# Kernel optimization log

Measured on AMD Instinct MI355X. Metric: run time of the kernel, lower is better.

The kernel has to match this reference:

```python
import jax, jax.numpy as jnp
import numpy as np

EPS = 1e-5
H = 12  # num_heads

def ste_sign(x):
    # forward: sign(x) in {-1,+1}; backward: grad passes where |x|<1 (clip STE)
    c = jnp.clip(x, -1.0, 1.0)
    s = jnp.where(x >= 0, 1.0, -1.0).astype(x.dtype)
    return c + jax.lax.stop_gradient(s - c)

def bin_w(w):
    # adaptive per-output-channel scaling: alpha = mean|w| (detached), weight = alpha*sign(w)
    alpha = jax.lax.stop_gradient(jnp.mean(jnp.abs(w), axis=1, keepdims=True))
    return alpha * ste_sign(w)

def layernorm(x, g, b):
    mu = jnp.mean(x, axis=-1, keepdims=True)
    var = jnp.var(x, axis=-1, keepdims=True)
    return (x - mu) * jax.lax.rsqrt(var + EPS) * g + b

def setup_inputs():
    key = jax.random.key(0)
    ks = jax.random.split(key, 6)
    B, N, C, hid = 8, 1024, 768, 3072
    s = 0.02
    return {
        "x": jax.random.normal(ks[0], (B, N, C), jnp.float32),
        "ln1_g": jnp.ones((C,), jnp.float32),
        "ln1_b": jnp.zeros((C,), jnp.float32),
        "w_qkv": jax.random.normal(ks[1], (3 * C, C), jnp.float32) * s,
        "w_proj": jax.random.normal(ks[2], (C, C), jnp.float32) * s,
        "b_proj": jnp.zeros((C,), jnp.float32),
        "ls1_g": 1e-5 * jnp.ones((C,), jnp.float32),
        "ln2_g": jnp.ones((C,), jnp.float32),
        "ln2_b": jnp.zeros((C,), jnp.float32),
        "w_fc1": jax.random.normal(ks[3], (hid, C), jnp.float32) * s,
        "b_fc1": jnp.zeros((hid,), jnp.float32),
        "w_fc2": jax.random.normal(ks[4], (C, hid), jnp.float32) * s,
        "b_fc2": jnp.zeros((C,), jnp.float32),
        "ls2_g": 1e-5 * jnp.ones((C,), jnp.float32),
    }

def reference(x, ln1_g, ln1_b, w_qkv, w_proj, b_proj, ls1_g, ln2_g, ln2_b, w_fc1, b_fc1, w_fc2, b_fc2, ls2_g):
    B, N, C = x.shape
    hd = C // H
    scale = hd ** -0.5
    # --- binarized attention ---
    h = layernorm(x, ln1_g, ln1_b)
    qkv = jnp.einsum('bnc,oc->bno', ste_sign(h), bin_w(w_qkv))        # 1w1a qkv proj
    qkv = qkv.reshape(B, N, 3, H, hd).transpose(2, 0, 3, 1, 4)        # [3,B,H,N,hd]
    bqkv = ste_sign(qkv)                                              # BinaryQuantizer
    q, k, v = bqkv[0], bqkv[1], bqkv[2]
    attn = jnp.einsum('bhnd,bhmd->bhnm', q, k) * scale                # [B,H,N,N]
    sm = jax.nn.softmax(attn, axis=-1)
    abin = (attn > 0).astype(x.dtype)                                 # SoftmaxBinaryQuantizer fwd value
    attn_eff = sm + jax.lax.stop_gradient(abin - sm)                  # STE: fwd=binary, bwd=softmax
    o = jnp.einsum('bhnm,bhmd->bhnd', attn_eff, v)
    o = o.transpose(0, 2, 1, 3).reshape(B, N, C)
    o = jnp.einsum('bnc,oc->bno', ste_sign(o), bin_w(w_proj)) + b_proj
    x = x + ls1_g * o
    # --- binary MLP (1-bit weight, 32-bit activation) ---
    h2 = layernorm(x, ln2_g, ln2_b)
    m = jax.nn.gelu(jnp.einsum('bnc,hc->bnh', h2, bin_w(w_fc1)) + b_fc1, approximate=False)
    m = jnp.einsum('bnh,ch->bnc', m, bin_w(w_fc2)) + b_fc2
    return x + ls2_g * m
```

## Files before the change

### kernel.cpp

```cpp
#include <hip/hip_runtime.h>

#define NTOK 8192
#define CDIM 768
#define HIDD 3072
#define NQKV 2304
#define SEQL 1024
#define NHEAD 12

typedef int i32x4 __attribute__((ext_vector_type(4)));
typedef float f32x4 __attribute__((ext_vector_type(4)));
typedef signed char sc16 __attribute__((ext_vector_type(16)));
typedef unsigned short us4 __attribute__((ext_vector_type(4)));

__device__ __forceinline__ unsigned short f32_to_bf16(float f) {
    unsigned int u = __float_as_uint(f);
    u += 0x7FFFu + ((u >> 16) & 1u);
    return (unsigned short)(u >> 16);
}
__device__ __forceinline__ float bf16_to_f32(unsigned short h) {
    return __uint_as_float(((unsigned)h) << 16);
}

__device__ __forceinline__ void gload_lds16(const void* g, void* l) {
    __builtin_amdgcn_global_load_lds(
        (const __attribute__((address_space(1))) unsigned int*)g,
        (__attribute__((address_space(3))) unsigned int*)l, 16, 0, 0);
}

__device__ __forceinline__ void sign_alpha_row(
    const float* __restrict__ w, signed char* __restrict__ ws,
    float* __restrict__ alpha, int K, bool perm, int row, float* red)
{
    const float* wr = w + (size_t)row * K;
    signed char* wsr = ws + (size_t)row * K;
    float s = 0.f;
    for (int i = threadIdx.x; i < K; i += 256) {
        float v = wr[i];
        int ip = perm ? ((i & ~63) | (((i & 15) << 2) | ((i >> 4) & 3))) : i;
        wsr[ip] = (v >= 0.f) ? 1 : -1;
        s += fabsf(v);
    }
    if (alpha) {
        for (int off = 32; off > 0; off >>= 1) s += __shfl_down(s, off);
        if ((threadIdx.x & 63) == 0) red[threadIdx.x >> 6] = s;
        __syncthreads();
        if (threadIdx.x == 0) alpha[row] = (red[0] + red[1] + red[2] + red[3]) / (float)K;
    }
}

__global__ void __launch_bounds__(256) prep_front(
    const float* __restrict__ w_qkv, signed char* __restrict__ wqkv_s,
    const float* __restrict__ x, const float* __restrict__ ln1_g,
    const float* __restrict__ ln1_b, signed char* __restrict__ a1,
    unsigned short* __restrict__ xb16)
{
    const int blk = blockIdx.x;
    __shared__ float red[8];

    if (blk < 2304) {
        sign_alpha_row(w_qkv, wqkv_s, nullptr, CDIM, false, blk, red);
        return;
    }
    int row = blk - 2304;
    const float* xr = x + (size_t)row * CDIM;
    float v0 = xr[threadIdx.x], v1 = xr[threadIdx.x + 256], v2 = xr[threadIdx.x + 512];
    unsigned short* xbrow = xb16 + (size_t)row * CDIM;
    xbrow[threadIdx.x]       = f32_to_bf16(v0);
    xbrow[threadIdx.x + 256] = f32_to_bf16(v1);
    xbrow[threadIdx.x + 512] = f32_to_bf16(v2);
    float s = v0 + v1 + v2, s2 = v0 * v0 + v1 * v1 + v2 * v2;
    for (int off = 32; off > 0; off >>= 1) { s += __shfl_down(s, off); s2 += __shfl_down(s2, off); }
    if ((threadIdx.x & 63) == 0) { red[threadIdx.x >> 6] = s; red[4 + (threadIdx.x >> 6)] = s2; }
    __syncthreads();
    float ts = red[0] + red[1] + red[2] + red[3];
    float t2 = red[4] + red[5] + red[6] + red[7];
    float mu = ts * (1.0f / CDIM);
    float var = t2 * (1.0f / CDIM) - mu * mu;
    float rstd = rsqrtf(var + 1e-5f);
    signed char* orow = a1 + (size_t)row * CDIM;
    float vv[3] = {v0, v1, v2};
#pragma unroll
    for (int p = 0; p < 3; p++) {
        int i = threadIdx.x + p * 256;
        float val = (vv[p] - mu) * rstd * ln1_g[i] + ln1_b[i];
        orow[i] = (val >= 0.f) ? 1 : -1;
    }
}

__global__ void __launch_bounds__(256) ln2q_kernel(const unsigned short* __restrict__ x, const float* __restrict__ g,
                                                   const float* __restrict__ b, signed char* __restrict__ out,
                                                   float* __restrict__ rowscale) {
    int row = blockIdx.x;
    const unsigned short* xr = x + (size_t)row * CDIM;
    float v0 = bf16_to_f32(xr[threadIdx.x]);
    float v1 = bf16_to_f32(xr[threadIdx.x + 256]);
    float v2 = bf16_to_f32(xr[threadIdx.x + 512]);
    float s = v0 + v1 + v2, s2 = v0 * v0 + v1 * v1 + v2 * v2;
    for (int off = 32; off > 0; off >>= 1) { s += __shfl_down(s, off); s2 += __shfl_down(s2, off); }
    __shared__ float red[8];
    __shared__ float redm[4];
    if ((threadIdx.x & 63) == 0) { red[threadIdx.x >> 6] = s; red[4 + (threadIdx.x >> 6)] = s2; }
    __syncthreads();
    float ts = red[0] + red[1] + red[2] + red[3];
    float t2 = red[4] + red[5] + red[6] + red[7];
    float mu = ts * (1.0f / CDIM);
    float var = t2 * (1.0f / CDIM) - mu * mu;
    float rstd = rsqrtf(var + 1e-5f);
    float a0 = (v0 - mu) * rstd * g[threadIdx.x] + b[threadIdx.x];
    float a1 = (v1 - mu) * rstd * g[threadIdx.x + 256] + b[threadIdx.x + 256];
    float a2v = (v2 - mu) * rstd * g[threadIdx.x + 512] + b[threadIdx.x + 512];
    float mx = fmaxf(fabsf(a0), fmaxf(fabsf(a1), fabsf(a2v)));
    for (int off = 32; off > 0; off >>= 1) mx = fmaxf(mx, __shfl_down(mx, off));
    if ((threadIdx.x & 63) == 0) redm[threadIdx.x >> 6] = mx;
    __syncthreads();
    float rmax = fmaxf(fmaxf(redm[0], redm[1]), fmaxf(redm[2], redm[3]));
    rmax = fmaxf(rmax, 1e-20f);
    float inv = 127.f / rmax;
    signed char* orow = out + (size_t)row * CDIM;
    orow[threadIdx.x]       = (signed char)__float2int_rn(a0 * inv);
    orow[threadIdx.x + 256] = (signed char)__float2int_rn(a1 * inv);
    orow[threadIdx.x + 512] = (signed char)__float2int_rn(a2v * inv);
    if (threadIdx.x == 0) rowscale[row] = rmax * (1.f / 127.f);
}

enum { EPI_GELU = 2, EPI_QKV = 3 };
#define MSCALE_INV 16.0f

template<int EPI>
__global__ void __launch_bounds__(512, 4) gemm_i8(
    const signed char* __restrict__ A, const signed char* __restrict__ B,
    int M, int N, int K,
    const float* __restrict__ alpha, const float* __restrict__ bias,
    const float* __restrict__ rowscale,
    signed char* __restrict__ outB, signed char* __restrict__ vtB)
{
    __shared__ __align__(16) char lds_raw[3 * (256 + 128) * 64];
    auto As = (signed char (*)[256][64])lds_raw;
    auto Bs = (signed char (*)[128][64])(lds_raw + 3 * 256 * 64);

    const int tid = threadIdx.x, ln = tid & 63, w = tid >> 6;
    const int wm = w >> 1, wn = w & 1;
    const int lq = ln & 15, khi = ln >> 4;

    const int nwg = gridDim.x * gridDim.y;
    const int id = blockIdx.y * gridDim.x + blockIdx.x;
    const int nid = (id & 7) * (nwg >> 3) + (id >> 3);
    const int bxs = nid % gridDim.x, bys = nid / gridDim.x;
    const int bm = bys * 256, bn = bxs * 128;

    const i32x4 iz = {0, 0, 0, 0};
    i32x4 acc[4][4];
#pragma unroll
    for (int m = 0; m < 4; m++)
#pragma unroll
        for (int n = 0; n < 4; n++) acc[m][n] = iz;

    const int srow = tid >> 2, scol = (tid & 3) * 16;
    const int ssrc = ((tid & 3) ^ ((srow >> 1) & 3)) * 16;
    const int sa = 16 * (khi ^ ((lq >> 1) & 3));

    auto STAGE = [&](int p, int k0) {
        gload_lds16(A + (size_t)(bm + srow) * K + k0 + ssrc, &As[p][srow][scol]);
        gload_lds16(A + (size_t)(bm + 128 + srow) * K + k0 + ssrc, &As[p][128 + srow][scol]);
        gload_lds16(B + (size_t)(bn + srow) * K + k0 + ssrc, &Bs[p][srow][scol]);
    };
    auto COMPUTE = [&](int p, bool prefetch, int knext) {
        i32x4 aF[4], bF[4];
#pragma unroll
        for (int m = 0; m < 4; m++) aF[m] = *(const i32x4*)&As[p][wm * 64 + m * 16 + lq][sa];
#pragma unroll
        for (int n = 0; n < 4; n++) bF[n] = *(const i32x4*)&Bs[p][wn * 64 + n * 16 + lq][sa];
        if (prefetch) STAGE((p + 2) % 3, knext);
        __builtin_amdgcn_s_setprio(1);
#pragma unroll
        for (int m = 0; m < 4; m++)
#pragma unroll
            for (int n = 0; n < 4; n++)
                acc[m][n] = __builtin_amdgcn_mfma_i32_16x16x64_i8(aF[m], bF[n], acc[m][n], 0, 0, 0);
        __builtin_amdgcn_s_setprio(0);
    };

    const int nst = K >> 6;
    STAGE(0, 0);
    STAGE(1, 64);
#pragma unroll 1
    for (int t = 0; t < nst - 1; t++) {
        asm volatile("s_waitcnt vmcnt(3)" ::: "memory");
        asm volatile("s_waitcnt lgkmcnt(0)" ::: "memory");
        __builtin_amdgcn_s_barrier();
        COMPUTE(t % 3, t + 2 < nst, (t + 2) << 6);
    }
    asm volatile("s_waitcnt vmcnt(0)" ::: "memory");
    asm volatile("s_waitcnt lgkmcnt(0)" ::: "memory");
    __builtin_amdgcn_s_barrier();
    COMPUTE((nst - 1) % 3, false, 0);

    const int r0 = bm + wm * 64;
    const int c0 = bn + wn * 64;

    if constexpr (EPI == EPI_GELU) {
        float al[4], bi[4];
#pragma unroll
        for (int n = 0; n < 4; n++) {
            al[n] = alpha[c0 + n * 16 + lq];
            bi[n] = bias[c0 + n * 16 + lq];
        }
#pragma unroll
        for (int m = 0; m < 4; m++)
#pragma unroll
            for (int i = 0; i < 4; i++) {
                int r = r0 + m * 16 + khi * 4 + i;
                float rs = rowscale[r];
                unsigned pk = 0;
#pragma unroll
                for (int n = 0; n < 4; n++) {
                    float t = al[n] * ((float)acc[m][n][i] * rs) + bi[n];
                    float y2 = 1.5957691f * t + 0.07135481f * t * t * t;
                    float ge = t * __builtin_amdgcn_rcpf(1.0f + __expf(-y2));
                    float qf = fminf(fmaxf(ge * MSCALE_INV, -127.f), 127.f);
                    pk |= (unsigned)(unsigned char)(signed char)__float2int_rn(qf) << (8 * n);
                }
                *(unsigned*)(outB + (size_t)r * N + c0 + lq * 4) = pk;
            }
    } else {
        if (c0 < 1536) {
#pragma unroll
            for (int m = 0; m < 4; m++)
#pragma unroll
                for (int i = 0; i < 4; i++) {
                    int r = r0 + m * 16 + khi * 4 + i;
                    unsigned pk = 0;
#pragma unroll
                    for (int n = 0; n < 4; n++)
                        pk |= (unsigned)(unsigned char)(signed char)((acc[m][n][i] >= 0) ? 1 : -1) << (8 * n);
                    *(unsigned*)(outB + (size_t)r * 1536 + c0 + lq * 4) = pk;
                }
        } else {
#pragma unroll
            for (int m = 0; m < 4; m++)
#pragma unroll
                for (int n = 0; n < 4; n++) {
                    int cg = c0 + n * 16 + lq - 1536;
                    int hh = cg >> 6, dd = cg & 63;
                    int rb = r0 + m * 16 + khi * 4;
                    unsigned pk = 0;
#pragma unroll
                    for (int i = 0; i < 4; i++)
                        pk |= (unsigned)(unsigned char)(signed char)((acc[m][n][i] >= 0) ? 1 : -1) << (8 * i);
                    *(unsigned*)(vtB + (((size_t)(rb >> 10) * NHEAD + hh) * 64 + dd) * SEQL + (rb & 1023)) = pk;
                }
        }
    }
}

template<bool OUTF32>
__global__ void __launch_bounds__(256) gemm_resid(
    const signed char* __restrict__ A, const signed char* __restrict__ B,
    int N, int K,
    const float* __restrict__ alpha, const float* __restrict__ bias,
    const float* __restrict__ ls, const unsigned short* __restrict__ residH,
    float ascale,
    float* __restrict__ outF, unsigned short* __restrict__ outH)
{
    __shared__ __align__(16) char lds_raw[3 * (128 + 64) * 64];
    auto As = (signed char (*)[128][64])lds_raw;
    auto Bs = (signed char (*)[64][64])(lds_raw + 3 * 128 * 64);

    const int tid = threadIdx.x, ln = tid & 63, w = tid >> 6;
    const int wm = w >> 1, wn = w & 1;
    const int lq = ln & 15, khi = ln >> 4;

    const int nwg = gridDim.x * gridDim.y;
    const int id = blockIdx.y * gridDim.x + blockIdx.x;
    const int nid = (id & 7) * (nwg >> 3) + (id >> 3);
    const int bxs = nid % gridDim.x, bys = nid / gridDim.x;
    const int bm = bys * 128, bn = bxs * 64;

    const int erow = tid >> 4;
    const int ec4 = (tid & 15) * 4;
    f32x4 a4 = *(const f32x4*)&alpha[bn + ec4];
    f32x4 b4 = *(const f32x4*)&bias[bn + ec4];
    f32x4 l4 = *(const f32x4*)&ls[bn + ec4];
    us4 rH[8];
#pragma unroll
    for (int p = 0; p < 8; p++) {
        size_t g = (size_t)(bm + p * 16 + erow) * N + bn + ec4;
        rH[p] = *(const us4*)&residH[g];
    }

    const i32x4 iz = {0, 0, 0, 0};
    i32x4 acc[4][2];
#pragma unroll
    for (int m = 0; m < 4; m++)
#pragma unroll
        for (int n = 0; n < 2; n++) acc[m][n] = iz;

    const int srow = tid >> 2, scol = (tid & 3) * 16;
    const int ssrc = ((tid & 3) ^ ((srow >> 1) & 3)) * 16;
    const int sa = 16 * (khi ^ ((lq >> 1) & 3));

    auto STAGE = [&](int p, int k0) {
        gload_lds16(A + (size_t)(bm + srow) * K + k0 + ssrc, &As[p][srow][scol]);
        gload_lds16(A + (size_t)(bm + 64 + srow) * K + k0 + ssrc, &As[p][64 + srow][scol]);
        gload_lds16(B + (size_t)(bn + srow) * K + k0 + ssrc, &Bs[p][srow][scol]);
    };
    auto COMPUTE = [&](int p, bool prefetch, int knext) {
        i32x4 aF[4], bF[2];
#pragma unroll
        for (int m = 0; m < 4; m++) aF[m] = *(const i32x4*)&As[p][wm * 64 + m * 16 + lq][sa];
#pragma unroll
        for (int n = 0; n < 2; n++) bF[n] = *(const i32x4*)&Bs[p][wn * 32 + n * 16 + lq][sa];
        if (prefetch) STAGE((p + 2) % 3, knext);
        __builtin_amdgcn_s_setprio(1);
#pragma unroll
        for (int m = 0; m < 4; m++)
#pragma unroll
            for (int n = 0; n < 2; n++)
                acc[m][n] = __builtin_amdgcn_mfma_i32_16x16x64_i8(aF[m], bF[n], acc[m][n], 0, 0, 0);
        __builtin_amdgcn_s_setprio(0);
    };

    const int nst = K >> 6;
    STAGE(0, 0);
    STAGE(1, 64);
#pragma unroll 1
    for (int t = 0; t < nst - 1; t++) {
        asm volatile("s_waitcnt vmcnt(3)" ::: "memory");
        asm volatile("s_waitcnt lgkmcnt(0)" ::: "memory");
        __builtin_amdgcn_s_barrier();
        COMPUTE(t % 3, t + 2 < nst, (t + 2) << 6);
    }
    asm volatile("s_waitcnt vmcnt(0)" ::: "memory");
    asm volatile("s_waitcnt lgkmcnt(0)" ::: "memory");
    __builtin_amdgcn_s_barrier();
    COMPUTE((nst - 1) % 3, false, 0);

    __syncthreads();
    float (*Cf)[68] = (float (*)[68])lds_raw;
#pragma unroll
    for (int m = 0; m < 4; m++)
#pragma unroll
        for (int n = 0; n < 2; n++)
#pragma unroll
            for (int i = 0; i < 4; i++)
                Cf[wm * 64 + m * 16 + khi * 4 + i][wn * 32 + n * 16 + lq] =
                    (float)acc[m][n][i] * ascale;
    __syncthreads();
#pragma unroll
    for (int p = 0; p < 8; p++) {
        int row = p * 16 + erow;
        f32x4 v4 = *(const f32x4*)&Cf[row][ec4];
        size_t g = (size_t)(bm + row) * N + bn + ec4;
        f32x4 r;
        r.x = bf16_to_f32(rH[p].x); r.y = bf16_to_f32(rH[p].y);
        r.z = bf16_to_f32(rH[p].z); r.w = bf16_to_f32(rH[p].w);
        f32x4 o4 = r + l4 * (a4 * v4 + b4);
        if constexpr (OUTF32) {
            *(f32x4*)&outF[g] = o4;
        } else {
            us4 h;
            h.x = f32_to_bf16(o4.x); h.y = f32_to_bf16(o4.y);
            h.z = f32_to_bf16(o4.z); h.w = f32_to_bf16(o4.w);
            *(us4*)&outH[g] = h;
        }
    }
}

__global__ void __launch_bounds__(256) attn_prep(
    const signed char* __restrict__ qk, const signed char* __restrict__ vt,
    signed char* __restrict__ a2,
    const float* __restrict__ w_proj, const float* __restrict__ w_fc1,
    const float* __restrict__ w_fc2,
    signed char* __restrict__ wproj_s, signed char* __restrict__ wfc1_s,
    signed char* __restrict__ wfc2_s,
    float* __restrict__ a_proj, float* __restrict__ a_fc1, float* __restrict__ a_fc2)
{
    const int blk = blockIdx.x;
    if (blk >= 768) {
        __shared__ float red[4];
        if (blk < 1536)      sign_alpha_row(w_proj, wproj_s, a_proj, CDIM, true,  blk - 768, red);
        else if (blk < 4608) sign_alpha_row(w_fc1,  wfc1_s,  a_fc1,  CDIM, false, blk - 1536, red);
        else                 sign_alpha_row(w_fc2,  wfc2_s,  a_fc2,  HIDD, true,  blk - 4608, red);
        return;
    }

    const int id = blk;
    const int nid = (id & 7) * 96 + (id >> 3);
    const int bh = nid >> 3, qb = nid & 7;
    const int b = bh / NHEAD, h = bh % NHEAD;
    const int tid = threadIdx.x, ln = tid & 63, w = tid >> 6;
    const int lq = ln & 15, khi = ln >> 4;

    __shared__ signed char Ks[64][80];
    __shared__ signed char Vts[64][80];
    __shared__ signed char Pw[4][32][80];

    const size_t tokbase = (size_t)b * SEQL;
    const int q0 = qb * 128 + w * 32;
    const int str = tid >> 2, stc = (tid & 3) * 16;
    const size_t vtrow = ((size_t)bh * 64 + str) * SEQL;

    i32x4 qfrag[2];
#pragma unroll
    for (int qf = 0; qf < 2; qf++)
        qfrag[qf] = *(const i32x4*)(qk + (tokbase + q0 + qf * 16 + lq) * 1536 + h * 64 + khi * 16);

    const i32x4 iz = {0, 0, 0, 0};
    i32x4 o[2][4];
#pragma unroll
    for (int qf = 0; qf < 2; qf++)
#pragma unroll
        for (int df = 0; df < 4; df++) o[qf][df] = iz;

    auto LOADJ = [&](int j, sc16& kr, sc16& vr) {
        kr = *(const sc16*)(qk + (tokbase + j * 64 + str) * 1536 + 768 + h * 64 + stc);
        vr = *(const sc16*)(vt + vtrow + j * 64 + stc);
    };
    auto STORE = [&](const sc16& kr, const sc16& vr) {
        *(sc16*)&Ks[str][stc] = kr;
        *(sc16*)&Vts[str][stc] = vr;
    };
    auto COMPUTE = [&]() {
        i32x4 kfrag[4];
#pragma unroll
        for (int kf = 0; kf < 4; kf++)
            kfrag[kf] = *(const i32x4*)&Ks[kf * 16 + lq][khi * 16];
#pragma unroll
        for (int kf = 0; kf < 4; kf++) {
#pragma unroll
            for (int qf = 0; qf < 2; qf++) {
                i32x4 st = __builtin_amdgcn_mfma_i32_16x16x64_i8(kfrag[kf], qfrag[qf], iz, 0, 0, 0);
                unsigned pb = (st[0] > 0 ? 1u : 0u) | (st[1] > 0 ? 0x100u : 0u) |
                              (st[2] > 0 ? 0x10000u : 0u) | (st[3] > 0 ? 0x1000000u : 0u);
                *(unsigned*)&Pw[w][qf * 16 + lq][kf * 16 + khi * 4] = pb;
            }
        }
        i32x4 pa[2];
#pragma unroll
        for (int qf = 0; qf < 2; qf++)
            pa[qf] = *(const i32x4*)&Pw[w][qf * 16 + lq][khi * 16];
#pragma unroll
        for (int df = 0; df < 4; df++) {
            i32x4 vfr = *(const i32x4*)&Vts[df * 16 + lq][khi * 16];
#pragma unroll
            for (int qf = 0; qf < 2; qf++)
                o[qf][df] = __builtin_amdgcn_mfma_i32_16x16x64_i8(pa[qf], vfr, o[qf][df], 0, 0, 0);
        }
    };

    sc16 ka, va, kb, vb;
    LOADJ(0, ka, va);
#pragma unroll 1
    for (int jj = 0; jj < 16; jj += 2) {
        __syncthreads();
        STORE(ka, va);
        __syncthreads();
        LOADJ(jj + 1, kb, vb);
        COMPUTE();
        __syncthreads();
        STORE(kb, vb);
        __syncthreads();
        if (jj + 2 < 16) LOADJ(jj + 2, ka, va);
        COMPUTE();
    }

#pragma unroll
    for (int qf = 0; qf < 2; qf++)
#pragma unroll
        for (int i = 0; i < 4; i++) {
            int qrow = q0 + qf * 16 + khi * 4 + i;
            unsigned pk = 0;
#pragma unroll
            for (int df = 0; df < 4; df++)
                pk |= (unsigned)(unsigned char)(signed char)((o[qf][df][i] >= 0) ? 1 : -1) << (8 * df);
            *(unsigned*)(a2 + (tokbase + qrow) * CDIM + h * 64 + lq * 4) = pk;
        }
}

static const size_t OFF_WQKV  = 0;
static const size_t OFF_WPROJ = 1769472;
static const size_t OFF_WFC1  = 2359296;
static const size_t OFF_WFC2  = 4718592;
static const size_t OFF_APROJ = 7077888;
static const size_t OFF_AFC1  = 7080960;
static const size_t OFF_AFC2  = 7093248;
static const size_t OFF_H2SC  = 7096320;
static const size_t OFF_QK    = 7129088;
static const size_t OFF_VT    = 19712000;
static const size_t OFF_A1    = 26003456;
static const size_t OFF_A2    = 32294912;
static const size_t OFF_M1    = 38586368;
static const size_t OFF_H2    = 63752192;
static const size_t OFF_X1B   = OFF_QK;
static const size_t OFF_XB16  = OFF_M1;

extern "C" void kernel_launch(void* const* d_in, const int* in_sizes, int n_in,
                              void* d_out, int out_size, void* d_ws, size_t ws_size,
                              hipStream_t stream) {
    const float* x      = (const float*)d_in[0];
    const float* ln1_g  = (const float*)d_in[1];
    const float* ln1_b  = (const float*)d_in[2];
    const float* w_qkv  = (const float*)d_in[3];
    const float* w_proj = (const float*)d_in[4];
    const float* b_proj = (const float*)d_in[5];
    const float* ls1_g  = (const float*)d_in[6];
    const float* ln2_g  = (const float*)d_in[7];
    const float* ln2_b  = (const float*)d_in[8];
    const float* w_fc1  = (const float*)d_in[9];
    const float* b_fc1  = (const float*)d_in[10];
    const float* w_fc2  = (const float*)d_in[11];
    const float* b_fc2  = (const float*)d_in[12];
    const float* ls2_g  = (const float*)d_in[13];
    float* out = (float*)d_out;

    char* ws = (char*)d_ws;
    signed char* wqkv_s  = (signed char*)(ws + OFF_WQKV);
    signed char* wproj_s = (signed char*)(ws + OFF_WPROJ);
    signed char* wfc1_s  = (signed char*)(ws + OFF_WFC1);
    signed char* wfc2_s  = (signed char*)(ws + OFF_WFC2);
    float* a_proj  = (float*)(ws + OFF_APROJ);
    float* a_fc1   = (float*)(ws + OFF_AFC1);
    float* a_fc2   = (float*)(ws + OFF_AFC2);
    float* h2scale = (float*)(ws + OFF_H2SC);
    signed char* qk   = (signed char*)(ws + OFF_QK);
    signed char* vt   = (signed char*)(ws + OFF_VT);
    signed char* a1   = (signed char*)(ws + OFF_A1);
    signed char* a2   = (signed char*)(ws + OFF_A2);
    signed char* m1   = (signed char*)(ws + OFF_M1);
    signed char* h2   = (signed char*)(ws + OFF_H2);
    unsigned short* x1b  = (unsigned short*)(ws + OFF_X1B);
    unsigned short* xb16 = (unsigned short*)(ws + OFF_XB16);

    prep_front<<<2304 + NTOK, 256, 0, stream>>>(w_qkv, wqkv_s, x, ln1_g, ln1_b, a1, xb16);

    gemm_i8<EPI_QKV><<<dim3(NQKV / 128, NTOK / 256), 512, 0, stream>>>(
        a1, wqkv_s, NTOK, NQKV, CDIM, nullptr, nullptr, nullptr, qk, vt);

    attn_prep<<<5376, 256, 0, stream>>>(qk, vt, a2,
                                        w_proj, w_fc1, w_fc2,
                                        wproj_s, wfc1_s, wfc2_s,
                                        a_proj, a_fc1, a_fc2);

    gemm_resid<false><<<dim3(CDIM / 64, NTOK / 128), 256, 0, stream>>>(
        a2, wproj_s, CDIM, CDIM, a_proj, b_proj, ls1_g, xb16, 1.0f, nullptr, x1b);

    ln2q_kernel<<<NTOK, 256, 0, stream>>>(x1b, ln2_g, ln2_b, h2, h2scale);

    gemm_i8<EPI_GELU><<<dim3(HIDD / 128, NTOK / 256), 512, 0, stream>>>(
        h2, wfc1_s, NTOK, HIDD, CDIM, a_fc1, b_fc1, h2scale, m1, nullptr);

    gemm_resid<true><<<dim3(CDIM / 64, NTOK / 128), 256, 0, stream>>>(
        m1, wfc2_s, CDIM, HIDD, a_fc2, b_fc2, ls2_g, x1b, 1.0f / MSCALE_INV, out, nullptr);
}
```

Before: 157.2 us.

## Shrink int8 GEMM tiles to 128x128 with 256 threads and vectorize layernorm kernels

The int8 GEMM used for the QKV and FC1 projections moves from 256x128 tiles with 512 threads to 128x128 tiles with 256 threads. This halves LDS use and doubles the number of workgroups, which is meant to improve occupancy and balance across the CUs at some cost in operand reuse. The two layernorm/quantize kernels now use 192 active threads doing 4-wide vector loads and packed stores instead of scalar byte accesses. Each change is meant to cut memory instruction count, but the vector loads and stores leave a quarter of each block idle.

```diff
diff --git a/kernel.cpp b/kernel.cpp
--- a/kernel.cpp
+++ b/kernel.cpp
@@ -62,28 +62,40 @@
         return;
     }
     int row = blk - 2304;
+    const int t = threadIdx.x;
+    const bool act = t < 192;
     const float* xr = x + (size_t)row * CDIM;
-    float v0 = xr[threadIdx.x], v1 = xr[threadIdx.x + 256], v2 = xr[threadIdx.x + 512];
-    unsigned short* xbrow = xb16 + (size_t)row * CDIM;
-    xbrow[threadIdx.x]       = f32_to_bf16(v0);
-    xbrow[threadIdx.x + 256] = f32_to_bf16(v1);
-    xbrow[threadIdx.x + 512] = f32_to_bf16(v2);
-    float s = v0 + v1 + v2, s2 = v0 * v0 + v1 * v1 + v2 * v2;
+    f32x4 xv = {0.f, 0.f, 0.f, 0.f};
+    if (act) xv = *(const f32x4*)&xr[t * 4];
+    if (act) {
+        us4 h;
+        h.x = f32_to_bf16(xv.x); h.y = f32_to_bf16(xv.y);
+        h.z = f32_to_bf16(xv.z); h.w = f32_to_bf16(xv.w);
+        *(us4*)&xb16[(size_t)row * CDIM + t * 4] = h;
+    }
+    float s = xv.x + xv.y + xv.z + xv.w;
+    float s2 = xv.x * xv.x + xv.y * xv.y + xv.z * xv.z + xv.w * xv.w;
     for (int off = 32; off > 0; off >>= 1) { s += __shfl_down(s, off); s2 += __shfl_down(s2, off); }
-    if ((threadIdx.x & 63) == 0) { red[threadIdx.x >> 6] = s; red[4 + (threadIdx.x >> 6)] = s2; }
+    if ((t & 63) == 0) { red[t >> 6] = s; red[4 + (t >> 6)] = s2; }
     __syncthreads();
     float ts = red[0] + red[1] + red[2] + red[3];
     float t2 = red[4] + red[5] + red[6] + red[7];
     float mu = ts * (1.0f / CDIM);
     float var = t2 * (1.0f / CDIM) - mu * mu;
     float rstd = rsqrtf(var + 1e-5f);
-    signed char* orow = a1 + (size_t)row * CDIM;
-    float vv[3] = {v0, v1, v2};
-#pragma unroll
-    for (int p = 0; p < 3; p++) {
-        int i = threadIdx.x + p * 256;
-        float val = (vv[p] - mu) * rstd * ln1_g[i] + ln1_b[i];
-        orow[i] = (val >= 0.f) ? 1 : -1;
+    if (act) {
+        f32x4 g4 = *(const f32x4*)&ln1_g[t * 4];
+        f32x4 b4 = *(const f32x4*)&ln1_b[t * 4];
+        unsigned pk = 0;
+        float v[4] = {xv.x, xv.y, xv.z, xv.w};
+        float gg[4] = {g4.x, g4.y, g4.z, g4.w};
+        float bb[4] = {b4.x, b4.y, b4.z, b4.w};
+#pragma unroll
+        for (int e = 0; e < 4; e++) {
+            float val = (v[e] - mu) * rstd * gg[e] + bb[e];
+            pk |= (unsigned)(unsigned char)(signed char)((val >= 0.f) ? 1 : -1) << (8 * e);
+        }
+        *(unsigned*)(a1 + (size_t)row * CDIM + t * 4) = pk;
     }
 }
 
@@ -91,52 +103,69 @@
                                                    const float* __restrict__ b, signed char* __restrict__ out,
                                                    float* __restrict__ rowscale) {
     int row = blockIdx.x;
-    const unsigned short* xr = x + (size_t)row * CDIM;
-    float v0 = bf16_to_f32(xr[threadIdx.x]);
-    float v1 = bf16_to_f32(xr[threadIdx.x + 256]);
-    float v2 = bf16_to_f32(xr[threadIdx.x + 512]);
-    float s = v0 + v1 + v2, s2 = v0 * v0 + v1 * v1 + v2 * v2;
+    const int t = threadIdx.x;
+    const bool act = t < 192;
+    float v[4] = {0.f, 0.f, 0.f, 0.f};
+    if (act) {
+        us4 xv = *(const us4*)&x[(size_t)row * CDIM + t * 4];
+        v[0] = bf16_to_f32(xv.x); v[1] = bf16_to_f32(xv.y);
+        v[2] = bf16_to_f32(xv.z); v[3] = bf16_to_f32(xv.w);
+    }
+    float s = v[0] + v[1] + v[2] + v[3];
+    float s2 = v[0] * v[0] + v[1] * v[1] + v[2] * v[2] + v[3] * v[3];
     for (int off = 32; off > 0; off >>= 1) { s += __shfl_down(s, off); s2 += __shfl_down(s2, off); }
     __shared__ float red[8];
     __shared__ float redm[4];
-    if ((threadIdx.x & 63) == 0) { red[threadIdx.x >> 6] = s; red[4 + (threadIdx.x >> 6)] = s2; }
+    if ((t & 63) == 0) { red[t >> 6] = s; red[4 + (t >> 6)] = s2; }
     __syncthreads();
     float ts = red[0] + red[1] + red[2] + red[3];
     float t2 = red[4] + red[5] + red[6] + red[7];
     float mu = ts * (1.0f / CDIM);
     float var = t2 * (1.0f / CDIM) - mu * mu;
     float rstd = rsqrtf(var + 1e-5f);
-    float a0 = (v0 - mu) * rstd * g[threadIdx.x] + b[threadIdx.x];
-    float a1 = (v1 - mu) * rstd * g[threadIdx.x + 256] + b[threadIdx.x + 256];
-    float a2v = (v2 - mu) * rstd * g[threadIdx.x + 512] + b[threadIdx.x + 512];
-    float mx = fmaxf(fabsf(a0), fmaxf(fabsf(a1), fabsf(a2v)));
+    float a[4] = {0.f, 0.f, 0.f, 0.f};
+    float mx = 0.f;
+    if (act) {
+        f32x4 g4 = *(const f32x4*)&g[t * 4];
+        f32x4 b4 = *(const f32x4*)&b[t * 4];
+        float gg[4] = {g4.x, g4.y, g4.z, g4.w};
+        float bb[4] = {b4.x, b4.y, b4.z, b4.w};
+#pragma unroll
+        for (int e = 0; e < 4; e++) {
+            a[e] = (v[e] - mu) * rstd * gg[e] + bb[e];
+            mx = fmaxf(mx, fabsf(a[e]));
+        }
+    }
     for (int off = 32; off > 0; off >>= 1) mx = fmaxf(mx, __shfl_down(mx, off));
-    if ((threadIdx.x & 63) == 0) redm[threadIdx.x >> 6] = mx;
+    if ((t & 63) == 0) redm[t >> 6] = mx;
     __syncthreads();
     float rmax = fmaxf(fmaxf(redm[0], redm[1]), fmaxf(redm[2], redm[3]));
     rmax = fmaxf(rmax, 1e-20f);
     float inv = 127.f / rmax;
-    signed char* orow = out + (size_t)row * CDIM;
-    orow[threadIdx.x]       = (signed char)__float2int_rn(a0 * inv);
-    orow[threadIdx.x + 256] = (signed char)__float2int_rn(a1 * inv);
-    orow[threadIdx.x + 512] = (signed char)__float2int_rn(a2v * inv);
-    if (threadIdx.x == 0) rowscale[row] = rmax * (1.f / 127.f);
+    if (act) {
+        unsigned pk = 0;
+#pragma unroll
+        for (int e = 0; e < 4; e++)
+            pk |= (unsigned)(unsigned char)(signed char)__float2int_rn(a[e] * inv) << (8 * e);
+        *(unsigned*)(out + (size_t)row * CDIM + t * 4) = pk;
+    }
+    if (t == 0) rowscale[row] = rmax * (1.f / 127.f);
 }
 
 enum { EPI_GELU = 2, EPI_QKV = 3 };
 #define MSCALE_INV 16.0f
 
 template<int EPI>
-__global__ void __launch_bounds__(512, 4) gemm_i8(
+__global__ void __launch_bounds__(256) gemm_i8(
     const signed char* __restrict__ A, const signed char* __restrict__ B,
-    int M, int N, int K,
+    int N, int K,
     const float* __restrict__ alpha, const float* __restrict__ bias,
     const float* __restrict__ rowscale,
     signed char* __restrict__ outB, signed char* __restrict__ vtB)
 {
-    __shared__ __align__(16) char lds_raw[3 * (256 + 128) * 64];
-    auto As = (signed char (*)[256][64])lds_raw;
-    auto Bs = (signed char (*)[128][64])(lds_raw + 3 * 256 * 64);
+    __shared__ __align__(16) char lds_raw[3 * 256 * 64];
+    auto As = (signed char (*)[128][64])lds_raw;
+    auto Bs = (signed char (*)[128][64])(lds_raw + 3 * 128 * 64);
 
     const int tid = threadIdx.x, ln = tid & 63, w = tid >> 6;
     const int wm = w >> 1, wn = w & 1;
@@ -146,7 +175,7 @@
     const int id = blockIdx.y * gridDim.x + blockIdx.x;
     const int nid = (id & 7) * (nwg >> 3) + (id >> 3);
     const int bxs = nid % gridDim.x, bys = nid / gridDim.x;
-    const int bm = bys * 256, bn = bxs * 128;
+    const int bm = bys * 128, bn = bxs * 128;
 
     const i32x4 iz = {0, 0, 0, 0};
     i32x4 acc[4][4];
@@ -161,8 +190,9 @@
 
     auto STAGE = [&](int p, int k0) {
         gload_lds16(A + (size_t)(bm + srow) * K + k0 + ssrc, &As[p][srow][scol]);
-        gload_lds16(A + (size_t)(bm + 128 + srow) * K + k0 + ssrc, &As[p][128 + srow][scol]);
+        gload_lds16(A + (size_t)(bm + 64 + srow) * K + k0 + ssrc, &As[p][64 + srow][scol]);
         gload_lds16(B + (size_t)(bn + srow) * K + k0 + ssrc, &Bs[p][srow][scol]);
+        gload_lds16(B + (size_t)(bn + 64 + srow) * K + k0 + ssrc, &Bs[p][64 + srow][scol]);
     };
     auto COMPUTE = [&](int p, bool prefetch, int knext) {
         i32x4 aF[4], bF[4];
@@ -185,7 +215,7 @@
     STAGE(1, 64);
 #pragma unroll 1
     for (int t = 0; t < nst - 1; t++) {
-        asm volatile("s_waitcnt vmcnt(3)" ::: "memory");
+        asm volatile("s_waitcnt vmcnt(4)" ::: "memory");
         asm volatile("s_waitcnt lgkmcnt(0)" ::: "memory");
         __builtin_amdgcn_s_barrier();
         COMPUTE(t % 3, t + 2 < nst, (t + 2) << 6);
@@ -533,8 +563,8 @@
 
     prep_front<<<2304 + NTOK, 256, 0, stream>>>(w_qkv, wqkv_s, x, ln1_g, ln1_b, a1, xb16);
 
-    gemm_i8<EPI_QKV><<<dim3(NQKV / 128, NTOK / 256), 512, 0, stream>>>(
-        a1, wqkv_s, NTOK, NQKV, CDIM, nullptr, nullptr, nullptr, qk, vt);
+    gemm_i8<EPI_QKV><<<dim3(NQKV / 128, NTOK / 128), 256, 0, stream>>>(
+        a1, wqkv_s, NQKV, CDIM, nullptr, nullptr, nullptr, qk, vt);
 
     attn_prep<<<5376, 256, 0, stream>>>(qk, vt, a2,
                                         w_proj, w_fc1, w_fc2,
@@ -546,8 +576,8 @@
 
     ln2q_kernel<<<NTOK, 256, 0, stream>>>(x1b, ln2_g, ln2_b, h2, h2scale);
 
-    gemm_i8<EPI_GELU><<<dim3(HIDD / 128, NTOK / 256), 512, 0, stream>>>(
-        h2, wfc1_s, NTOK, HIDD, CDIM, a_fc1, b_fc1, h2scale, m1, nullptr);
+    gemm_i8<EPI_GELU><<<dim3(HIDD / 128, NTOK / 128), 256, 0, stream>>>(
+        h2, wfc1_s, HIDD, CDIM, a_fc1, b_fc1, h2scale, m1, nullptr);
 
     gemm_resid<true><<<dim3(CDIM / 64, NTOK / 128), 256, 0, stream>>>(
         m1, wfc2_s, CDIM, HIDD, a_fc2, b_fc2, ls2_g, x1b, 1.0f / MSCALE_INV, out, nullptr);
```

After: 158.9 us. No clear change (+1.1%).
